# Performance work log

Hardware: AMD Instinct MI355X
Metric: run time of the kernel (lower is better)

The kernel has to match this reference:

```python
import jax, jax.numpy as jnp
import numpy as np

B, S, D, H = 4, 4096, 1024, 16
DH = D // H  # 64
EPS = 1e-6


def setup_inputs() -> dict:
    key = jax.random.key(0)
    ks = jax.random.split(key, 6)
    scale = 1.0 / np.sqrt(D).astype(np.float32)
    x = jax.random.normal(ks[0], (B, S, D), jnp.float32)
    # packed cache: rows 0..DH-1 = KV state S0, row DH = normalizer z0 (kept positive)
    state_cache = jax.random.uniform(ks[1], (B, H, DH + 1, DH), jnp.float32)
    Wq = jax.random.normal(ks[2], (D, D), jnp.float32) * scale
    Wk = jax.random.normal(ks[3], (D, D), jnp.float32) * scale
    Wv = jax.random.normal(ks[4], (D, D), jnp.float32) * scale
    Wo = jax.random.normal(ks[5], (D, D), jnp.float32) * scale
    return {"x": x, "state_cache": state_cache, "Wq": Wq, "Wk": Wk, "Wv": Wv, "Wo": Wo}


def reference(x, state_cache, Wq, Wk, Wv, Wo):
    b, s, d = x.shape
    h, dh = H, d // H

    def heads(t):  # [b,s,d] -> [s,b,h,dh] (seq-major for scan)
        return t.reshape(b, s, h, dh).transpose(1, 0, 2, 3)

    phi = lambda t: jax.nn.elu(t) + 1.0  # positive feature map
    q = phi(heads(x @ Wq))
    k = phi(heads(x @ Wk))
    v = heads(x @ Wv)

    S0 = state_cache[:, :, :dh, :]   # [b,h,dh,dh]
    z0 = state_cache[:, :, dh, :]    # [b,h,dh]

    def step(carry, inp):
        Sst, z = carry
        qt, kt, vt = inp  # each [b,h,dh]
        Sst = Sst + jnp.einsum('bhd,bhe->bhde', kt, vt)
        z = z + kt
        num = jnp.einsum('bhd,bhde->bhe', qt, Sst)            # [b,h,dh]
        den = jnp.einsum('bhd,bhd->bh', qt, z)[..., None]     # [b,h,1]
        return (Sst, z), num / (den + EPS)

    _, outs = jax.lax.scan(step, (S0, z0), (q, k, v))  # outs: [s,b,h,dh]
    out = outs.transpose(1, 0, 2, 3).reshape(b, s, d)
    return out @ Wo
```

## Files before the change

### kernel.cpp

```cpp
#include <hip/hip_runtime.h>

#define B_ 4
#define S_ 4096
#define D_ 1024
#define H_ 16
#define DH 64
#define CHUNK 64
#define NC (S_ / CHUNK)
#define BH (B_ * H_)
#define STATE_N 4160
#define EPS 1e-6f

typedef __bf16 bf16;
typedef __bf16 bf16x8 __attribute__((ext_vector_type(8)));
typedef __bf16 bf16x4 __attribute__((ext_vector_type(4)));
typedef float v4f __attribute__((ext_vector_type(4)));

#define MFMA16(a, b, c) __builtin_amdgcn_mfma_f32_16x16x32_bf16(a, b, c, 0, 0, 0)

__device__ __forceinline__ void load_lds16(const bf16* g, bf16* l) {
  __builtin_amdgcn_global_load_lds(
      (const __attribute__((address_space(1))) unsigned int*)g,
      (__attribute__((address_space(3))) unsigned int*)l, 16, 0, 0);
}

__global__ __launch_bounds__(256) void cvt_f32_bf16(const float* __restrict__ in,
                                                    bf16* __restrict__ out) {
  const size_t i = ((size_t)blockIdx.x * 256 + threadIdx.x) * 8;
  float4 a = *(const float4*)(in + i);
  float4 b = *(const float4*)(in + i + 4);
  bf16x8 o;
  o[0] = (bf16)a.x; o[1] = (bf16)a.y; o[2] = (bf16)a.z; o[3] = (bf16)a.w;
  o[4] = (bf16)b.x; o[5] = (bf16)b.y; o[6] = (bf16)b.z; o[7] = (bf16)b.w;
  *(bf16x8*)(out + i) = o;
}

__global__ __launch_bounds__(256) void transpose_w4(
    const float* __restrict__ w0, const float* __restrict__ w1,
    const float* __restrict__ w2, const float* __restrict__ w3,
    bf16* __restrict__ out) {
  __shared__ float tile[32][33];
  const int z = blockIdx.z;
  const float* in = (z == 0) ? w0 : (z == 1) ? w1 : (z == 2) ? w2 : w3;
  bf16* o = out + (size_t)z * D_ * D_;
  const int bx = blockIdx.x * 32, by = blockIdx.y * 32;
  const int tx = threadIdx.x & 31, ty = threadIdx.x >> 5;
#pragma unroll
  for (int i = 0; i < 32; i += 8)
    tile[ty + i][tx] = in[(size_t)(by + ty + i) * D_ + bx + tx];
  __syncthreads();
#pragma unroll
  for (int i = 0; i < 32; i += 8)
    o[(size_t)(bx + ty + i) * D_ + by + tx] = (bf16)tile[tx][ty + i];
}

__global__ __launch_bounds__(256) void gemm_nt(const bf16* __restrict__ A,
                                               const bf16* __restrict__ BT,
                                               bf16* __restrict__ Cb,
                                               float* __restrict__ Cf, int act) {
  constexpr int TM = 128, TN = 128, BK = 32;
  constexpr int CLD = 132;
  __shared__ __align__(16) char smem[32 * CLD * 4];
  bf16* Al = (bf16*)smem;
  bf16* Bl = (bf16*)(smem + 8192);
  float* Cl = (float*)smem;

  const int tid = threadIdx.x;
  const int wave = tid >> 6, lane = tid & 63;
  const int quad = lane >> 4, l16 = lane & 15;
  const int bm = blockIdx.x * TM, bn = blockIdx.y * TN;
  const int wm = (wave & 1) * 64, wn = (wave >> 1) * 64;

  const int srow = wave * 16 + (lane >> 2);
  const int sgrp = lane & 3;
  const bf16* gA0 = A + (size_t)(bm + srow) * D_ + sgrp * 8;
  const bf16* gA1 = gA0 + (size_t)64 * D_;
  const bf16* gB0 = BT + (size_t)(bn + srow) * D_ + sgrp * 8;
  const bf16* gB1 = gB0 + (size_t)64 * D_;
  bf16* lA0 = Al + wave * 16 * BK;
  bf16* lA1 = lA0 + 64 * BK;
  bf16* lB0 = Bl + wave * 16 * BK;
  bf16* lB1 = lB0 + 64 * BK;

  v4f zero = {0.f, 0.f, 0.f, 0.f};
  v4f acc[4][4];
#pragma unroll
  for (int i = 0; i < 4; i++)
#pragma unroll
    for (int j = 0; j < 4; j++) acc[i][j] = zero;

  for (int k0 = 0; k0 < D_; k0 += BK) {
    __syncthreads();
    load_lds16(gA0 + k0, lA0);
    load_lds16(gA1 + k0, lA1);
    load_lds16(gB0 + k0, lB0);
    load_lds16(gB1 + k0, lB1);
    __syncthreads();
    bf16x8 af[4], bfr[4];
#pragma unroll
    for (int i = 0; i < 4; i++)
      af[i] = *(const bf16x8*)&Al[(wm + i * 16 + l16) * BK + quad * 8];
#pragma unroll
    for (int j = 0; j < 4; j++)
      bfr[j] = *(const bf16x8*)&Bl[(wn + j * 16 + l16) * BK + quad * 8];
#pragma unroll
    for (int i = 0; i < 4; i++)
#pragma unroll
      for (int j = 0; j < 4; j++) acc[i][j] = MFMA16(af[i], bfr[j], acc[i][j]);
  }

  const int lr = (wave & 1) * 16 + quad * 4;
  const int rrow = tid >> 3;
  const int rseg = (tid & 7) * 16;
  const int grow = bm + (rrow >> 4) * 64 + (rrow & 15);
#pragma unroll
  for (int i = 0; i < 4; i++) {
    __syncthreads();
#pragma unroll
    for (int j = 0; j < 4; j++) {
      const int col = wn + j * 16 + l16;
#pragma unroll
      for (int r = 0; r < 4; r++) {
        float x = acc[i][j][r];
        if (act) x = x > 0.f ? x + 1.f : __expf(x);
        Cl[(lr + r) * CLD + col] = x;
      }
    }
    __syncthreads();
    const float* src = &Cl[rrow * CLD + rseg];
    if (Cf) {
      float* dst = Cf + (size_t)(grow + i * 16) * D_ + bn + rseg;
#pragma unroll
      for (int u = 0; u < 4; u++)
        *(float4*)(dst + u * 4) = *(const float4*)(src + u * 4);
    } else {
      bf16x8 o0, o1;
#pragma unroll
      for (int u = 0; u < 8; u++) { o0[u] = (bf16)src[u]; o1[u] = (bf16)src[8 + u]; }
      bf16* dst = Cb + (size_t)(grow + i * 16) * D_ + bn + rseg;
      *(bf16x8*)dst = o0;
      *(bf16x8*)(dst + 8) = o1;
    }
  }
}

__global__ __launch_bounds__(256) void chunk_kv(const bf16* __restrict__ kb,
                                                const bf16* __restrict__ vb,
                                                float* __restrict__ states) {
  constexpr int LD = 88;
  __shared__ bf16 Kl[CHUNK * LD];
  __shared__ bf16 Vl[CHUNK * LD];
  const int tid = threadIdx.x;
  const int c = blockIdx.x, bh = blockIdx.y;
  const int b = bh >> 4, h = bh & 15;
  const size_t gbase = ((size_t)(b * S_ + c * CHUNK)) * D_ + h * DH;
#pragma unroll
  for (int rep = 0; rep < 2; rep++) {
    int flat = tid + rep * 256;
    int r = flat >> 3, sg = (flat & 7) * 8;
    *(bf16x8*)&Kl[r * LD + sg] = *(const bf16x8*)(kb + gbase + (size_t)r * D_ + sg);
    *(bf16x8*)&Vl[r * LD + sg] = *(const bf16x8*)(vb + gbase + (size_t)r * D_ + sg);
  }
  __syncthreads();
  const int d0 = (tid >> 4) * 4, e0 = (tid & 15) * 4;
  float acc[4][4] = {};
  for (int t = 0; t < CHUNK; t++) {
    bf16x4 k4 = *(const bf16x4*)&Kl[t * LD + d0];
    bf16x4 v4 = *(const bf16x4*)&Vl[t * LD + e0];
    float kf[4], vf[4];
#pragma unroll
    for (int i = 0; i < 4; i++) { kf[i] = (float)k4[i]; vf[i] = (float)v4[i]; }
#pragma unroll
    for (int i = 0; i < 4; i++)
#pragma unroll
      for (int j = 0; j < 4; j++) acc[i][j] += kf[i] * vf[j];
  }
  float* out = states + ((size_t)bh * NC + c) * STATE_N;
#pragma unroll
  for (int i = 0; i < 4; i++)
#pragma unroll
    for (int j = 0; j < 4; j++) out[(d0 + i) * 64 + (e0 + j)] = acc[i][j];
  if (tid < 64) {
    float zs = 0.f;
    for (int t = 0; t < CHUNK; t++) zs += (float)Kl[t * LD + tid];
    out[4096 + tid] = zs;
  }
}

__global__ __launch_bounds__(256) void state_prefix(const float* __restrict__ sc,
                                                    float* __restrict__ states) {
  const int bh = blockIdx.x;
  const int e = blockIdx.y * 256 + threadIdx.x;
  if (e >= STATE_N) return;
  const float* scb = sc + (size_t)bh * (DH + 1) * DH;
  float run = scb[e];
  float* p = states + (size_t)bh * NC * STATE_N + e;
  for (int c = 0; c < NC; c++) {
    float tmp = p[(size_t)c * STATE_N];
    p[(size_t)c * STATE_N] = run;
    run += tmp;
  }
}

__global__ __launch_bounds__(256) void attn_pass2(
    const bf16* __restrict__ qb, const bf16* __restrict__ kb,
    const bf16* __restrict__ vb, const float* __restrict__ states,
    bf16* __restrict__ ao) {
  constexpr int LD = 88;
  __shared__ bf16 Ql[CHUNK * LD];
  __shared__ bf16 Kl[CHUNK * LD];
  __shared__ bf16 VT[DH * LD];
  __shared__ bf16 S0T[DH * LD];
  __shared__ bf16 Pl[CHUNK * LD];
  __shared__ float denl[CHUNK];
  __shared__ float z0l[DH];
  const int tid = threadIdx.x;
  const int wave = tid >> 6, lane = tid & 63;
  const int quad = lane >> 4, l16 = lane & 15;
  const int c = blockIdx.x, bh = blockIdx.y;
  const int b = bh >> 4, h = bh & 15;
  const size_t gbase = ((size_t)(b * S_ + c * CHUNK)) * D_ + h * DH;

#pragma unroll
  for (int rep = 0; rep < 2; rep++) {
    int flat = tid + rep * 256;
    int r = flat >> 3, sg = (flat & 7) * 8;
    *(bf16x8*)&Ql[r * LD + sg] = *(const bf16x8*)(qb + gbase + (size_t)r * D_ + sg);
    *(bf16x8*)&Kl[r * LD + sg] = *(const bf16x8*)(kb + gbase + (size_t)r * D_ + sg);
    bf16x8 vv = *(const bf16x8*)(vb + gbase + (size_t)r * D_ + sg);
#pragma unroll
    for (int u = 0; u < 8; u++) VT[(sg + u) * LD + r] = vv[u];
  }
  const float* st = states + ((size_t)bh * NC + c) * STATE_N;
  for (int f = tid; f < 4096; f += 256) S0T[(f & 63) * LD + (f >> 6)] = (bf16)st[f];
  if (tid < DH) z0l[tid] = st[4096 + tid];
  __syncthreads();

  v4f zero = {0.f, 0.f, 0.f, 0.f};
  v4f pacc[4];
#pragma unroll
  for (int j = 0; j < 4; j++) pacc[j] = zero;
#pragma unroll
  for (int ks = 0; ks < 2; ks++) {
    bf16x8 aq = *(const bf16x8*)&Ql[(wave * 16 + l16) * LD + ks * 32 + quad * 8];
#pragma unroll
    for (int j = 0; j < 4; j++) {
      bf16x8 bk = *(const bf16x8*)&Kl[(j * 16 + l16) * LD + ks * 32 + quad * 8];
      pacc[j] = MFMA16(aq, bk, pacc[j]);
    }
  }
  float rs[4] = {0.f, 0.f, 0.f, 0.f};
#pragma unroll
  for (int j = 0; j < 4; j++) {
#pragma unroll
    for (int r = 0; r < 4; r++) {
      int t = wave * 16 + quad * 4 + r;
      int col = j * 16 + l16;
      float p = (col <= t) ? pacc[j][r] : 0.f;
      Pl[t * LD + col] = (bf16)p;
      rs[r] += p;
    }
  }
#pragma unroll
  for (int m = 1; m < 16; m <<= 1)
#pragma unroll
    for (int r = 0; r < 4; r++) rs[r] += __shfl_xor(rs[r], m, 64);
  if (l16 == 0)
#pragma unroll
    for (int r = 0; r < 4; r++) denl[wave * 16 + quad * 4 + r] = rs[r];
  __syncthreads();
  if (tid < CHUNK) {
    float qz = 0.f;
    for (int d = 0; d < DH; d++) qz += (float)Ql[tid * LD + d] * z0l[d];
    denl[tid] += qz;
  }
  __syncthreads();

  v4f nacc[4];
#pragma unroll
  for (int j = 0; j < 4; j++) nacc[j] = zero;
#pragma unroll
  for (int ks = 0; ks < 2; ks++) {
    bf16x8 ap = *(const bf16x8*)&Pl[(wave * 16 + l16) * LD + ks * 32 + quad * 8];
#pragma unroll
    for (int j = 0; j < 4; j++) {
      bf16x8 bv = *(const bf16x8*)&VT[(j * 16 + l16) * LD + ks * 32 + quad * 8];
      nacc[j] = MFMA16(ap, bv, nacc[j]);
    }
  }
#pragma unroll
  for (int ks = 0; ks < 2; ks++) {
    bf16x8 aq = *(const bf16x8*)&Ql[(wave * 16 + l16) * LD + ks * 32 + quad * 8];
#pragma unroll
    for (int j = 0; j < 4; j++) {
      bf16x8 bs = *(const bf16x8*)&S0T[(j * 16 + l16) * LD + ks * 32 + quad * 8];
      nacc[j] = MFMA16(aq, bs, nacc[j]);
    }
  }
#pragma unroll
  for (int j = 0; j < 4; j++) {
#pragma unroll
    for (int r = 0; r < 4; r++) {
      int t = wave * 16 + quad * 4 + r;
      int e = j * 16 + l16;
      float o = nacc[j][r] / (denl[t] + EPS);
      ao[gbase + (size_t)t * D_ + e] = (bf16)o;
    }
  }
}

extern "C" void kernel_launch(void* const* d_in, const int* in_sizes, int n_in,
                              void* d_out, int out_size, void* d_ws, size_t ws_size,
                              hipStream_t stream) {
  const float* x  = (const float*)d_in[0];
  const float* sc = (const float*)d_in[1];
  const float* Wq = (const float*)d_in[2];
  const float* Wk = (const float*)d_in[3];
  const float* Wv = (const float*)d_in[4];
  const float* Wo = (const float*)d_in[5];
  float* out = (float*)d_out;

  const size_t MSZ = (size_t)B_ * S_ * D_;
  const size_t WSZ = (size_t)D_ * D_;
  bf16* xb = (bf16*)d_ws;
  bf16* qb = xb + MSZ;
  bf16* kb = qb + MSZ;
  bf16* vb = kb + MSZ;
  bf16* ao = vb + MSZ;
  bf16* wt = ao + MSZ;
  float* states = (float*)(wt + 4 * WSZ);

  cvt_f32_bf16<<<MSZ / (256 * 8), 256, 0, stream>>>(x, xb);
  transpose_w4<<<dim3(32, 32, 4), 256, 0, stream>>>(Wq, Wk, Wv, Wo, wt);

  dim3 ggrid(128, 8);
  gemm_nt<<<ggrid, 256, 0, stream>>>(xb, wt + 0 * WSZ, qb, nullptr, 1);
  gemm_nt<<<ggrid, 256, 0, stream>>>(xb, wt + 1 * WSZ, kb, nullptr, 1);
  gemm_nt<<<ggrid, 256, 0, stream>>>(xb, wt + 2 * WSZ, vb, nullptr, 0);

  chunk_kv<<<dim3(NC, BH), 256, 0, stream>>>(kb, vb, states);
  state_prefix<<<dim3(BH, 17), 256, 0, stream>>>(sc, states);
  attn_pass2<<<dim3(NC, BH), 256, 0, stream>>>(qb, kb, vb, states, ao);

  gemm_nt<<<ggrid, 256, 0, stream>>>(ao, wt + 3 * WSZ, nullptr, out, 0);
}
```

Baseline: 477.6 us.

## Double-buffer GEMM LDS tiles and fuse Q/K/V projections into one launch

The GEMM main loop now uses two LDS stages, so the next K-slice is loaded while the current one is computed, and each iteration needs one barrier instead of two. The three Q/K/V projection GEMMs are merged into one launch over a 128x24 grid. The blockIdx.y index selects the weight slice and output buffer, and activation is applied only for Q and K. LDS use doubles to 32KB per block, which may lower occupancy.

```diff
diff --git a/kernel.cpp b/kernel.cpp
--- a/kernel.cpp
+++ b/kernel.cpp
@@ -56,31 +56,31 @@
 
 __global__ __launch_bounds__(256) void gemm_nt(const bf16* __restrict__ A,
                                                const bf16* __restrict__ BT,
-                                               bf16* __restrict__ Cb,
-                                               float* __restrict__ Cf, int act) {
-  constexpr int TM = 128, TN = 128, BK = 32;
+                                               bf16* __restrict__ o0,
+                                               bf16* __restrict__ o1,
+                                               bf16* __restrict__ o2,
+                                               float* __restrict__ of) {
+  constexpr int TM = 128, BK = 32;
   constexpr int CLD = 132;
-  __shared__ __align__(16) char smem[32 * CLD * 4];
-  bf16* Al = (bf16*)smem;
-  bf16* Bl = (bf16*)(smem + 8192);
+  __shared__ __align__(16) char smem[32768];
   float* Cl = (float*)smem;
 
   const int tid = threadIdx.x;
   const int wave = tid >> 6, lane = tid & 63;
   const int quad = lane >> 4, l16 = lane & 15;
-  const int bm = blockIdx.x * TM, bn = blockIdx.y * TN;
+  const int bm = blockIdx.x * TM;
+  const int zz = blockIdx.y >> 3;
+  const int colg = (blockIdx.y & 7) * 128;
   const int wm = (wave & 1) * 64, wn = (wave >> 1) * 64;
+  const int act = (of == nullptr) && (zz < 2);
+  bf16* ob = (zz == 0) ? o0 : (zz == 1) ? o1 : o2;
 
   const int srow = wave * 16 + (lane >> 2);
   const int sgrp = lane & 3;
   const bf16* gA0 = A + (size_t)(bm + srow) * D_ + sgrp * 8;
   const bf16* gA1 = gA0 + (size_t)64 * D_;
-  const bf16* gB0 = BT + (size_t)(bn + srow) * D_ + sgrp * 8;
+  const bf16* gB0 = BT + ((size_t)blockIdx.y * 128 + srow) * D_ + sgrp * 8;
   const bf16* gB1 = gB0 + (size_t)64 * D_;
-  bf16* lA0 = Al + wave * 16 * BK;
-  bf16* lA1 = lA0 + 64 * BK;
-  bf16* lB0 = Bl + wave * 16 * BK;
-  bf16* lB1 = lB0 + 64 * BK;
 
   v4f zero = {0.f, 0.f, 0.f, 0.f};
   v4f acc[4][4];
@@ -89,24 +89,41 @@
 #pragma unroll
     for (int j = 0; j < 4; j++) acc[i][j] = zero;
 
-  for (int k0 = 0; k0 < D_; k0 += BK) {
+  auto stage = [&](int ks, int s) {
+    bf16* As = (bf16*)(smem + s * 16384);
+    bf16* Bs = As + 4096;
+    const int ko = ks * BK;
+    load_lds16(gA0 + ko, As + wave * 16 * BK);
+    load_lds16(gA1 + ko, As + (64 + wave * 16) * BK);
+    load_lds16(gB0 + ko, Bs + wave * 16 * BK);
+    load_lds16(gB1 + ko, Bs + (64 + wave * 16) * BK);
+  };
+  auto compute = [&](int s) {
+    const bf16* As = (const bf16*)(smem + s * 16384);
+    const bf16* Bs = As + 4096;
+    bf16x8 af[4], bfr[4];
+#pragma unroll
+    for (int i = 0; i < 4; i++)
+      af[i] = *(const bf16x8*)&As[(wm + i * 16 + l16) * BK + quad * 8];
+#pragma unroll
+    for (int j = 0; j < 4; j++)
+      bfr[j] = *(const bf16x8*)&Bs[(wn + j * 16 + l16) * BK + quad * 8];
+#pragma unroll
+    for (int i = 0; i < 4; i++)
+#pragma unroll
+      for (int j = 0; j < 4; j++) acc[i][j] = MFMA16(af[i], bfr[j], acc[i][j]);
+  };
+
+  constexpr int NK = D_ / BK;
+  stage(0, 0);
+  __syncthreads();
+  for (int k = 0; k < NK; k += 2) {
+    if (k + 1 < NK) stage(k + 1, 1);
+    compute(0);
     __syncthreads();
-    load_lds16(gA0 + k0, lA0);
-    load_lds16(gA1 + k0, lA1);
-    load_lds16(gB0 + k0, lB0);
-    load_lds16(gB1 + k0, lB1);
+    if (k + 2 < NK) stage(k + 2, 0);
+    compute(1);
     __syncthreads();
-    bf16x8 af[4], bfr[4];
-#pragma unroll
-    for (int i = 0; i < 4; i++)
-      af[i] = *(const bf16x8*)&Al[(wm + i * 16 + l16) * BK + quad * 8];
-#pragma unroll
-    for (int j = 0; j < 4; j++)
-      bfr[j] = *(const bf16x8*)&Bl[(wn + j * 16 + l16) * BK + quad * 8];
-#pragma unroll
-    for (int i = 0; i < 4; i++)
-#pragma unroll
-      for (int j = 0; j < 4; j++) acc[i][j] = MFMA16(af[i], bfr[j], acc[i][j]);
   }
 
   const int lr = (wave & 1) * 16 + quad * 4;
@@ -128,18 +145,18 @@
     }
     __syncthreads();
     const float* src = &Cl[rrow * CLD + rseg];
-    if (Cf) {
-      float* dst = Cf + (size_t)(grow + i * 16) * D_ + bn + rseg;
+    if (of) {
+      float* dst = of + (size_t)(grow + i * 16) * D_ + colg + rseg;
 #pragma unroll
       for (int u = 0; u < 4; u++)
         *(float4*)(dst + u * 4) = *(const float4*)(src + u * 4);
     } else {
-      bf16x8 o0, o1;
-#pragma unroll
-      for (int u = 0; u < 8; u++) { o0[u] = (bf16)src[u]; o1[u] = (bf16)src[8 + u]; }
-      bf16* dst = Cb + (size_t)(grow + i * 16) * D_ + bn + rseg;
-      *(bf16x8*)dst = o0;
-      *(bf16x8*)(dst + 8) = o1;
+      bf16x8 q0, q1;
+#pragma unroll
+      for (int u = 0; u < 8; u++) { q0[u] = (bf16)src[u]; q1[u] = (bf16)src[8 + u]; }
+      bf16* dst = ob + (size_t)(grow + i * 16) * D_ + colg + rseg;
+      *(bf16x8*)dst = q0;
+      *(bf16x8*)(dst + 8) = q1;
     }
   }
 }
@@ -333,14 +350,12 @@
   cvt_f32_bf16<<<MSZ / (256 * 8), 256, 0, stream>>>(x, xb);
   transpose_w4<<<dim3(32, 32, 4), 256, 0, stream>>>(Wq, Wk, Wv, Wo, wt);
 
-  dim3 ggrid(128, 8);
-  gemm_nt<<<ggrid, 256, 0, stream>>>(xb, wt + 0 * WSZ, qb, nullptr, 1);
-  gemm_nt<<<ggrid, 256, 0, stream>>>(xb, wt + 1 * WSZ, kb, nullptr, 1);
-  gemm_nt<<<ggrid, 256, 0, stream>>>(xb, wt + 2 * WSZ, vb, nullptr, 0);
+  gemm_nt<<<dim3(128, 24), 256, 0, stream>>>(xb, wt, qb, kb, vb, nullptr);
 
   chunk_kv<<<dim3(NC, BH), 256, 0, stream>>>(kb, vb, states);
   state_prefix<<<dim3(BH, 17), 256, 0, stream>>>(sc, states);
   attn_pass2<<<dim3(NC, BH), 256, 0, stream>>>(qb, kb, vb, states, ao);
 
-  gemm_nt<<<ggrid, 256, 0, stream>>>(ao, wt + 3 * WSZ, nullptr, out, 0);
-}
+  gemm_nt<<<dim3(128, 8), 256, 0, stream>>>(ao, wt + 3 * WSZ, nullptr, nullptr,
+                                            nullptr, out);
+}
```

Result: faster. 433.5 us (-9.2%).
